# Optimization experiments

Measured on AMD Instinct MI355X. Metric: run time of the kernel, lower is better.

Reference implementation:

```python
import jax, jax.numpy as jnp
import numpy as np

L = 6  # num_objects (greedy iterations)
BIG = 1e8  # penalty for already-used template ids (matches torch code)


def setup_inputs() -> dict:
    key = jax.random.key(0)
    k1, k2, k3, k4 = jax.random.split(key, 4)
    B, T, C, H, W = 16, 144, 1, 128, 128
    x = jax.random.uniform(k1, (B, C, H, W), jnp.float32)
    templates = jax.random.uniform(k2, (B, T, C, H, W), jnp.float32)
    masks = jax.random.uniform(k3, (B, T, 1, H, W), jnp.float32)
    background = jax.random.uniform(k4, (1, C, H, W), jnp.float32)
    return {"x": x, "templates": templates, "masks": masks, "background": background}


def _greedy_select(x, templates, masks, background):
    """Greedy template selection. Faithful to DecompModel._greedy_selection
    (use_empty is falsy by default -> empty template = 5*ones, empty mask = ones).
    Key identity used for efficiency: dead-leaves composition of the l
    already-selected objects is affine in whatever lies below them:
        recons = A + Mprod * below,
    where A accumulates painted objects and Mprod = prod(1 - mask_i).
    The new candidate at step l is painted BELOW the existing selection
    (it sits at the last index, and compose_templates paints last->first),
    so below = cand*cand_mask + bg*(1-cand_mask). Identical math, no
    O(B*T*l) recomposition per step."""
    B, T = templates.shape[0], templates.shape[1]
    H, W = templates.shape[-2], templates.shape[-1]
    empty_t = 5.0 * jnp.ones((B, 1) + templates.shape[2:], templates.dtype)
    empty_m = jnp.ones((B, 1) + masks.shape[2:], masks.dtype)
    temps = jnp.concatenate([empty_t, templates], axis=1)   # (B,T+1,C,H,W)
    ms = jnp.concatenate([empty_m, masks], axis=1)           # (B,T+1,1,H,W)
    bg = jnp.broadcast_to(background, (B,) + background.shape[1:])  # (B,C,H,W)

    A0 = jnp.zeros_like(bg)                                  # painted-so-far
    M0 = jnp.ones((B, 1, H, W), bg.dtype)                    # transmission
    used0 = jnp.zeros((B, T + 1), bool)
    bidx = jnp.arange(B)

    def step(carry, _):
        A, Mprod, used = carry
        below = temps * ms + bg[:, None] * (1.0 - ms)        # (B,T+1,C,H,W)
        recons = A[:, None] + Mprod[:, None] * below         # (B,T+1,C,H,W)
        errors = jnp.mean((x[:, None] - recons) ** 2, axis=(2, 3, 4))  # (B,T+1)
        errors = jnp.where(used, BIG, errors)
        ids = jnp.argmin(errors, axis=1)                     # (B,)
        hit = (jnp.arange(T + 1)[None, :] == ids[:, None]) & (ids[:, None] != 0)
        used = used | hit                                    # empty id=0 reusable
        sel_t = temps[bidx, ids]                             # (B,C,H,W)
        sel_m = ms[bidx, ids]                                # (B,1,H,W)
        A = A + Mprod * sel_t * sel_m
        Mprod = Mprod * (1.0 - sel_m)
        return (A, Mprod, used), ids

    (_, _, _), ids = jax.lax.scan(step, (A0, M0, used0), None, length=L)
    ids = ids.T                                              # (B,L)
    objects = temps[bidx[:, None], ids]                      # (B,L,C,H,W)
    omasks = ms[bidx[:, None], ids]                          # (B,L,1,H,W)
    return objects, omasks, ids


def _compose(objects, omasks, background):
    """Dead-leaves composition, painting from last object to first
    (first selected object ends up on top), as in compose_templates."""
    B, N = objects.shape[0], objects.shape[1]
    recons = jnp.broadcast_to(background, (B,) + background.shape[1:])
    for i in range(N):  # small fixed loop over L objects
        o = objects[:, N - 1 - i]
        m = omasks[:, N - 1 - i]
        recons = o * m + recons * (1.0 - m)
    return recons


def reference(x, templates, masks, background):
    objects, omasks, ids = _greedy_select(x, templates, masks, background)
    recons = _compose(objects, omasks, background)           # (B,C,H,W)
    return recons, objects, omasks, ids
```

## Files before the change

### kernel.cpp

```cpp
#include <hip/hip_runtime.h>

#define BB 16
#define TT 144
#define TP1 145
#define HWP 16384
#define HW4 4096
#define LL 6
#define BIGE 1e30

typedef float f4 __attribute__((ext_vector_type(4)));

static const size_t OFF_A     = 0;
static const size_t OFF_M     = 1048576;
static const size_t OFF_U     = 2097152;
static const size_t OFF_V     = 3145728;
static const size_t OFF_ERR   = 4194304;
static const size_t OFF_USED  = 4227072;
static const size_t OFF_BELOW = 4259840;
static const size_t WS_FULL   = OFF_BELOW + 150994944ull;

__device__ __forceinline__ float hsum(f4 v) { return ((v.x + v.y) + v.z) + v.w; }

__device__ __forceinline__ double blk_reduce(double s) {
    for (int off = 32; off; off >>= 1) s += __shfl_down(s, off);
    __shared__ double smr[4];
    if ((threadIdx.x & 63) == 0) smr[threadIdx.x >> 6] = s;
    __syncthreads();
    return smr[0] + smr[1] + smr[2] + smr[3];
}

__global__ void k_below_err0(const f4* __restrict__ temps, const f4* __restrict__ masks,
                             const f4* __restrict__ bg, const f4* __restrict__ x,
                             f4* __restrict__ below, double* __restrict__ err,
                             int* __restrict__ used) {
    const int t = blockIdx.x, b = blockIdx.y, tid = threadIdx.x;
    const f4* xb = x + (size_t)b * HW4;
    double s = 0.0;
    if (t == 0) {
        if (tid < TP1) used[b * TP1 + tid] = 0;
        for (int j = tid; j < HW4; j += 256) {
            f4 xv = xb[j];
            s += (double)(100.f - 10.f * hsum(xv));
        }
    } else {
        const size_t row = ((size_t)(b * TT + t - 1)) * HW4;
        for (int j = tid; j < HW4; j += 256) {
            f4 tv = __builtin_nontemporal_load(&temps[row + j]);
            f4 mv = __builtin_nontemporal_load(&masks[row + j]);
            f4 bv = bg[j], xv = xb[j];
            f4 w = tv * mv + bv * (1.f - mv);
            below[row + j] = w;
            f4 g = w * (w - 2.f * xv);
            s += (double)hsum(g);
        }
    }
    double tot = blk_reduce(s);
    if (tid == 0) err[b * TP1 + t] = tot;
}

template <int MODE>
__global__ void k_err(const f4* __restrict__ below,
                      const f4* __restrict__ temps, const f4* __restrict__ masks,
                      const f4* __restrict__ bg,
                      const f4* __restrict__ u, const f4* __restrict__ v,
                      const int* __restrict__ used, double* __restrict__ err) {
    const int t = blockIdx.x, b = blockIdx.y, tid = threadIdx.x;
    if (t != 0 && used[b * TP1 + t]) {
        if (tid == 0) err[b * TP1 + t] = BIGE;
        return;
    }
    const f4* ub = u + (size_t)b * HW4;
    const f4* vb = v + (size_t)b * HW4;
    double s = 0.0;
    if (t == 0) {
        for (int j = tid; j < HW4; j += 256) {
            f4 uu = ub[j], vv = vb[j];
            float g = 25.f * hsum(vv) - 10.f * hsum(uu);
            s += (double)g;
        }
    } else if (MODE == 0) {
        const size_t row = ((size_t)(b * TT + t - 1)) * HW4;
        for (int j = tid; j < HW4; j += 256) {
            f4 w = below[row + j], uu = ub[j], vv = vb[j];
            f4 g = w * (vv * w - 2.f * uu);
            s += (double)hsum(g);
        }
    } else {
        const size_t row = ((size_t)(b * TT + t - 1)) * HW4;
        for (int j = tid; j < HW4; j += 256) {
            f4 tv = temps[row + j], mv = masks[row + j], bv = bg[j];
            f4 uu = ub[j], vv = vb[j];
            f4 w = tv * mv + bv * (1.f - mv);
            f4 g = w * (vv * w - 2.f * uu);
            s += (double)hsum(g);
        }
    }
    double tot = blk_reduce(s);
    if (tid == 0) err[b * TP1 + t] = tot;
}

template <bool FIRST, bool LAST>
__global__ void k_upd(const f4* __restrict__ temps, const f4* __restrict__ masks,
                      const f4* __restrict__ x, const f4* __restrict__ bg,
                      const double* __restrict__ err,
                      int* __restrict__ used, f4* __restrict__ A, f4* __restrict__ M,
                      f4* __restrict__ u, f4* __restrict__ v,
                      f4* __restrict__ out_obj, f4* __restrict__ out_msk,
                      f4* __restrict__ out_rec, float* __restrict__ out_ids, int l) {
    const int tid = threadIdx.x;
    const int gid = blockIdx.x * 256 + tid;
    const int b = gid >> 12;
    const int p = gid & (HW4 - 1);
    __shared__ int ssel;
    if (tid < 64) {
        double best = 1e301;
        int bi = TP1;
        for (int t = tid; t < TP1; t += 64) {
            double e = err[b * TP1 + t];
            if (e < best) { best = e; bi = t; }
        }
        for (int off = 32; off; off >>= 1) {
            double oe = __shfl_down(best, off);
            int    oi = __shfl_down(bi, off);
            if (oe < best || (oe == best && oi < bi)) { best = oe; bi = oi; }
        }
        if (tid == 0) ssel = bi;
    }
    __syncthreads();
    const int id = ssel;
    f4 st, sm;
    if (id == 0) {
        st = (f4){5.f, 5.f, 5.f, 5.f};
        sm = (f4){1.f, 1.f, 1.f, 1.f};
    } else {
        size_t base = ((size_t)(b * TT + id - 1)) * HW4 + p;
        st = temps[base];
        sm = masks[base];
    }
    f4 a, mp;
    if (FIRST) { a = (f4){0.f, 0.f, 0.f, 0.f}; mp = (f4){1.f, 1.f, 1.f, 1.f}; }
    else       { a = A[gid]; mp = M[gid]; }
    a = a + mp * st * sm;
    mp = mp * (1.f - sm);
    const size_t ob = ((size_t)(b * LL + l)) * HW4 + p;
    out_obj[ob] = st;
    out_msk[ob] = sm;
    if (LAST) {
        out_rec[gid] = a + mp * bg[p];
    } else {
        A[gid] = a; M[gid] = mp;
        f4 xv = x[gid];
        u[gid] = (xv - a) * mp;
        v[gid] = mp * mp;
    }
    if ((blockIdx.x & 15) == 0 && tid == 0) {
        if (id != 0) used[b * TP1 + id] = 1;
        out_ids[b * LL + l] = (float)id;
    }
}

__global__ void k_uv0(const f4* __restrict__ x, f4* __restrict__ u, f4* __restrict__ v,
                      int* __restrict__ used) {
    int gid = blockIdx.x * blockDim.x + threadIdx.x;
    if (gid < BB * TP1) used[gid] = 0;
    if (gid >= BB * HW4) return;
    u[gid] = x[gid];
    v[gid] = (f4){1.f, 1.f, 1.f, 1.f};
}

static inline void launch_upd(bool first, bool last,
                              const f4* temps, const f4* masks, const f4* x, const f4* bg,
                              const double* err, int* used, f4* A, f4* M,
                              f4* u, f4* v, f4* out_obj, f4* out_msk, f4* out_rec,
                              float* out_ids, int l, hipStream_t stream) {
    if (first)
        k_upd<true, false><<<256, 256, 0, stream>>>(temps, masks, x, bg, err, used, A, M, u, v, out_obj, out_msk, out_rec, out_ids, l);
    else if (last)
        k_upd<false, true><<<256, 256, 0, stream>>>(temps, masks, x, bg, err, used, A, M, u, v, out_obj, out_msk, out_rec, out_ids, l);
    else
        k_upd<false, false><<<256, 256, 0, stream>>>(temps, masks, x, bg, err, used, A, M, u, v, out_obj, out_msk, out_rec, out_ids, l);
}

extern "C" void kernel_launch(void* const* d_in, const int* in_sizes, int n_in,
                              void* d_out, int out_size, void* d_ws, size_t ws_size,
                              hipStream_t stream) {
    const f4* x     = (const f4*)d_in[0];
    const f4* temps = (const f4*)d_in[1];
    const f4* masks = (const f4*)d_in[2];
    const f4* bg    = (const f4*)d_in[3];

    float* out      = (float*)d_out;
    f4*    out_rec  = (f4*)out;
    f4*    out_obj  = (f4*)(out + 262144);
    f4*    out_msk  = (f4*)(out + 262144 + 1572864);
    float* out_ids  = out + 262144 + 2 * 1572864;

    char* ws = (char*)d_ws;
    f4*     A     = (f4*)(ws + OFF_A);
    f4*     M     = (f4*)(ws + OFF_M);
    f4*     u     = (f4*)(ws + OFF_U);
    f4*     v     = (f4*)(ws + OFF_V);
    double* err   = (double*)(ws + OFF_ERR);
    int*    used  = (int*)(ws + OFF_USED);
    f4*     below = (f4*)(ws + OFF_BELOW);

    const bool full = (ws_size >= WS_FULL);

    if (full) {
        k_below_err0<<<dim3(TP1, BB), 256, 0, stream>>>(temps, masks, bg, x, below, err, used);
        for (int l = 0; l < LL; ++l) {
            launch_upd(l == 0, l == LL - 1, temps, masks, x, bg, err, used, A, M, u, v,
                       out_obj, out_msk, out_rec, out_ids, l, stream);
            if (l < LL - 1)
                k_err<0><<<dim3(TP1, BB), 256, 0, stream>>>(
                    below, nullptr, nullptr, nullptr, u, v, used, err);
        }
    } else {
        k_uv0<<<(BB * HW4 + 255) / 256, 256, 0, stream>>>(x, u, v, used);
        for (int l = 0; l < LL; ++l) {
            k_err<1><<<dim3(TP1, BB), 256, 0, stream>>>(
                nullptr, temps, masks, bg, u, v, used, err);
            launch_upd(l == 0, l == LL - 1, temps, masks, x, bg, err, used, A, M, u, v,
                       out_obj, out_msk, out_rec, out_ids, l, stream);
        }
    }
}
```

Baseline: 258.4 us.

## Store precomputed below in fp16 and refine near-best candidates in fp32

The cached per-candidate 'below' image is now stored as half precision, which halves the traffic of the per-step error sweep. A second kernel takes the fp16 error estimates and recomputes, in fp32 from the original templates and masks, only those candidates whose estimate lies within an error-bound margin of the minimum. All other candidates get a large sentinel, so selection should match the fp32 result as long as the margin bound holds. This adds one extra launch per step and depends on the heuristic margin being wide enough to keep the true argmin.

```diff
diff --git a/kernel.cpp b/kernel.cpp
--- a/kernel.cpp
+++ b/kernel.cpp
@@ -1,25 +1,35 @@
 #include <hip/hip_runtime.h>
+#include <math.h>
 
 #define BB 16
 #define TT 144
 #define TP1 145
 #define HWP 16384
 #define HW4 4096
+#define HW8 2048
 #define LL 6
 #define BIGE 1e30
 
-typedef float f4 __attribute__((ext_vector_type(4)));
+typedef float     f4 __attribute__((ext_vector_type(4)));
+typedef float     f8 __attribute__((ext_vector_type(8)));
+typedef _Float16  h4 __attribute__((ext_vector_type(4)));
+typedef _Float16  h8 __attribute__((ext_vector_type(8)));
 
 static const size_t OFF_A     = 0;
-static const size_t OFF_M     = 1048576;
-static const size_t OFF_U     = 2097152;
-static const size_t OFF_V     = 3145728;
-static const size_t OFF_ERR   = 4194304;
-static const size_t OFF_USED  = 4227072;
-static const size_t OFF_BELOW = 4259840;
-static const size_t WS_FULL   = OFF_BELOW + 150994944ull;
+static const size_t OFF_M     = 1u << 20;
+static const size_t OFF_U     = 2u << 20;
+static const size_t OFF_V     = 3u << 20;
+static const size_t OFF_ERR32 = 4u << 20;
+static const size_t OFF_ERR16 = (4u << 20) + 32768;
+static const size_t OFF_D     = (4u << 20) + 65536;
+static const size_t OFF_USED  = (4u << 20) + 81920;
+static const size_t OFF_B16   = (4u << 20) + 98304;
+static const size_t WS_FULL   = OFF_B16 + 75497472ull;
 
 __device__ __forceinline__ float hsum(f4 v) { return ((v.x + v.y) + v.z) + v.w; }
+__device__ __forceinline__ float hsum8(f8 v) {
+    return (((v.s0 + v.s1) + (v.s2 + v.s3)) + ((v.s4 + v.s5) + (v.s6 + v.s7)));
+}
 
 __device__ __forceinline__ double blk_reduce(double s) {
     for (int off = 32; off; off >>= 1) s += __shfl_down(s, off);
@@ -29,9 +39,18 @@
     return smr[0] + smr[1] + smr[2] + smr[3];
 }
 
+__device__ __forceinline__ void blk_reduce2(double& a, double& b) {
+    for (int off = 32; off; off >>= 1) { a += __shfl_down(a, off); b += __shfl_down(b, off); }
+    __shared__ double sa[4], sb[4];
+    if ((threadIdx.x & 63) == 0) { sa[threadIdx.x >> 6] = a; sb[threadIdx.x >> 6] = b; }
+    __syncthreads();
+    a = sa[0] + sa[1] + sa[2] + sa[3];
+    b = sb[0] + sb[1] + sb[2] + sb[3];
+}
+
 __global__ void k_below_err0(const f4* __restrict__ temps, const f4* __restrict__ masks,
                              const f4* __restrict__ bg, const f4* __restrict__ x,
-                             f4* __restrict__ below, double* __restrict__ err,
+                             h4* __restrict__ below16, double* __restrict__ err32,
                              int* __restrict__ used) {
     const int t = blockIdx.x, b = blockIdx.y, tid = threadIdx.x;
     const f4* xb = x + (size_t)b * HW4;
@@ -49,41 +68,115 @@
             f4 mv = __builtin_nontemporal_load(&masks[row + j]);
             f4 bv = bg[j], xv = xb[j];
             f4 w = tv * mv + bv * (1.f - mv);
-            below[row + j] = w;
+            below16[row + j] = __builtin_convertvector(w, h4);
             f4 g = w * (w - 2.f * xv);
             s += (double)hsum(g);
         }
     }
     double tot = blk_reduce(s);
-    if (tid == 0) err[b * TP1 + t] = tot;
-}
-
-template <int MODE>
-__global__ void k_err(const f4* __restrict__ below,
-                      const f4* __restrict__ temps, const f4* __restrict__ masks,
-                      const f4* __restrict__ bg,
-                      const f4* __restrict__ u, const f4* __restrict__ v,
-                      const int* __restrict__ used, double* __restrict__ err) {
+    if (tid == 0) err32[b * TP1 + t] = tot;
+}
+
+__global__ void k_err16(const h8* __restrict__ below16,
+                        const f4* __restrict__ u4, const f4* __restrict__ v4,
+                        const int* __restrict__ used, double* __restrict__ err16,
+                        double* __restrict__ D) {
     const int t = blockIdx.x, b = blockIdx.y, tid = threadIdx.x;
     if (t != 0 && used[b * TP1 + t]) {
-        if (tid == 0) err[b * TP1 + t] = BIGE;
-        return;
-    }
-    const f4* ub = u + (size_t)b * HW4;
-    const f4* vb = v + (size_t)b * HW4;
+        if (tid == 0) err16[b * TP1 + t] = BIGE;
+        return;
+    }
+    if (t == 0) {
+        const f4* ub = u4 + (size_t)b * HW4;
+        const f4* vb = v4 + (size_t)b * HW4;
+        double s = 0.0, d = 0.0;
+        for (int j = tid; j < HW4; j += 256) {
+            f4 uu = ub[j], vv = vb[j];
+            s += (double)(25.f * hsum(vv) - 10.f * hsum(uu));
+            f4 au = {fabsf(uu.x), fabsf(uu.y), fabsf(uu.z), fabsf(uu.w)};
+            d += (double)hsum(vv + au);
+        }
+        blk_reduce2(s, d);
+        if (tid == 0) { err16[b * TP1] = s; D[b] = d; }
+        return;
+    }
+    const f8* ub = (const f8*)(u4 + (size_t)b * HW4);
+    const f8* vb = (const f8*)(v4 + (size_t)b * HW4);
+    const h8* wb = below16 + ((size_t)(b * TT + t - 1)) * HW8;
+    double s = 0.0;
+    for (int j = tid; j < HW8; j += 256) {
+        f8 w = __builtin_convertvector(wb[j], f8);
+        f8 uu = ub[j], vv = vb[j];
+        f8 g = w * (vv * w - 2.f * uu);
+        s += (double)hsum8(g);
+    }
+    double tot = blk_reduce(s);
+    if (tid == 0) err16[b * TP1 + t] = tot;
+}
+
+__global__ void k_refine(const f4* __restrict__ temps, const f4* __restrict__ masks,
+                         const f4* __restrict__ bg,
+                         const f4* __restrict__ u4, const f4* __restrict__ v4,
+                         const double* __restrict__ err16, const double* __restrict__ D,
+                         double* __restrict__ err32) {
+    const int t = blockIdx.x, b = blockIdx.y, tid = threadIdx.x;
+    double e = (tid < TP1) ? err16[b * TP1 + tid] : 1e300;
+    for (int off = 32; off; off >>= 1) {
+        double oe = __shfl_down(e, off);
+        e = (oe < e) ? oe : e;
+    }
+    __shared__ double sm[4];
+    __shared__ double smin_s;
+    if ((tid & 63) == 0) sm[tid >> 6] = e;
+    __syncthreads();
+    if (tid == 0) {
+        double m0 = (sm[0] < sm[1]) ? sm[0] : sm[1];
+        double m1 = (sm[2] < sm[3]) ? sm[2] : sm[3];
+        smin_s = (m0 < m1) ? m0 : m1;
+    }
+    __syncthreads();
+    const double smin = smin_s;
+    const double mine = err16[b * TP1 + t];
+    const double margin = 2.0 * (1.0e-3 * D[b] + 0.25);
+    if (mine > smin + margin) {
+        if (tid == 0) err32[b * TP1 + t] = BIGE;
+        return;
+    }
+    if (t == 0) {
+        if (tid == 0) err32[b * TP1 + t] = mine;
+        return;
+    }
+    const f4* ub = u4 + (size_t)b * HW4;
+    const f4* vb = v4 + (size_t)b * HW4;
+    const size_t row = ((size_t)(b * TT + t - 1)) * HW4;
+    double s = 0.0;
+    for (int j = tid; j < HW4; j += 256) {
+        f4 tv = temps[row + j], mv = masks[row + j], bv = bg[j];
+        f4 uu = ub[j], vv = vb[j];
+        f4 w = tv * mv + bv * (1.f - mv);
+        f4 g = w * (vv * w - 2.f * uu);
+        s += (double)hsum(g);
+    }
+    double tot = blk_reduce(s);
+    if (tid == 0) err32[b * TP1 + t] = tot;
+}
+
+__global__ void k_err_f32(const f4* __restrict__ temps, const f4* __restrict__ masks,
+                          const f4* __restrict__ bg,
+                          const f4* __restrict__ u4, const f4* __restrict__ v4,
+                          const int* __restrict__ used, double* __restrict__ err32) {
+    const int t = blockIdx.x, b = blockIdx.y, tid = threadIdx.x;
+    if (t != 0 && used[b * TP1 + t]) {
+        if (tid == 0) err32[b * TP1 + t] = BIGE;
+        return;
+    }
+    const f4* ub = u4 + (size_t)b * HW4;
+    const f4* vb = v4 + (size_t)b * HW4;
     double s = 0.0;
     if (t == 0) {
         for (int j = tid; j < HW4; j += 256) {
             f4 uu = ub[j], vv = vb[j];
-            float g = 25.f * hsum(vv) - 10.f * hsum(uu);
-            s += (double)g;
-        }
-    } else if (MODE == 0) {
-        const size_t row = ((size_t)(b * TT + t - 1)) * HW4;
-        for (int j = tid; j < HW4; j += 256) {
-            f4 w = below[row + j], uu = ub[j], vv = vb[j];
-            f4 g = w * (vv * w - 2.f * uu);
-            s += (double)hsum(g);
+            s += (double)(25.f * hsum(vv) - 10.f * hsum(uu));
         }
     } else {
         const size_t row = ((size_t)(b * TT + t - 1)) * HW4;
@@ -96,7 +189,7 @@
         }
     }
     double tot = blk_reduce(s);
-    if (tid == 0) err[b * TP1 + t] = tot;
+    if (tid == 0) err32[b * TP1 + t] = tot;
 }
 
 template <bool FIRST, bool LAST>
@@ -200,27 +293,29 @@
     f4*     M     = (f4*)(ws + OFF_M);
     f4*     u     = (f4*)(ws + OFF_U);
     f4*     v     = (f4*)(ws + OFF_V);
-    double* err   = (double*)(ws + OFF_ERR);
+    double* err32 = (double*)(ws + OFF_ERR32);
+    double* err16 = (double*)(ws + OFF_ERR16);
+    double* D     = (double*)(ws + OFF_D);
     int*    used  = (int*)(ws + OFF_USED);
-    f4*     below = (f4*)(ws + OFF_BELOW);
+    h4*     b16   = (h4*)(ws + OFF_B16);
 
     const bool full = (ws_size >= WS_FULL);
 
     if (full) {
-        k_below_err0<<<dim3(TP1, BB), 256, 0, stream>>>(temps, masks, bg, x, below, err, used);
+        k_below_err0<<<dim3(TP1, BB), 256, 0, stream>>>(temps, masks, bg, x, b16, err32, used);
         for (int l = 0; l < LL; ++l) {
-            launch_upd(l == 0, l == LL - 1, temps, masks, x, bg, err, used, A, M, u, v,
+            launch_upd(l == 0, l == LL - 1, temps, masks, x, bg, err32, used, A, M, u, v,
                        out_obj, out_msk, out_rec, out_ids, l, stream);
-            if (l < LL - 1)
-                k_err<0><<<dim3(TP1, BB), 256, 0, stream>>>(
-                    below, nullptr, nullptr, nullptr, u, v, used, err);
+            if (l < LL - 1) {
+                k_err16<<<dim3(TP1, BB), 256, 0, stream>>>((const h8*)b16, u, v, used, err16, D);
+                k_refine<<<dim3(TP1, BB), 256, 0, stream>>>(temps, masks, bg, u, v, err16, D, err32);
+            }
         }
     } else {
         k_uv0<<<(BB * HW4 + 255) / 256, 256, 0, stream>>>(x, u, v, used);
         for (int l = 0; l < LL; ++l) {
-            k_err<1><<<dim3(TP1, BB), 256, 0, stream>>>(
-                nullptr, temps, masks, bg, u, v, used, err);
-            launch_upd(l == 0, l == LL - 1, temps, masks, x, bg, err, used, A, M, u, v,
+            k_err_f32<<<dim3(TP1, BB), 256, 0, stream>>>(temps, masks, bg, u, v, used, err32);
+            launch_upd(l == 0, l == LL - 1, temps, masks, x, bg, err32, used, A, M, u, v,
                        out_obj, out_msk, out_rec, out_ids, l, stream);
         }
     }
```

New measurement: 313.7 us. 21.4% more time.

## Fuse argmin and state update into per-candidate error kernel with ping-pong buffers

Applied to the files above, without the earlier changes.

Merges the separate update and error kernels into a single step kernel per greedy iteration. Every block redundantly recomputes the argmin over the previous errors and rebuilds A/M/u/v on the fly instead of reading stored u/v. The used-flag array is replaced by carrying the BIG sentinel forward in the error buffers, and A/M are double-buffered. The goal is fewer launches and less u/v traffic, paid for with redundant reads of the selected template and A/M in every candidate block. It also widens loads to 8-float vectors and remaps block order into chunks.

```diff
diff --git a/kernel.cpp b/kernel.cpp
--- a/kernel.cpp
+++ b/kernel.cpp
@@ -3,23 +3,26 @@
 #define BB 16
 #define TT 144
 #define TP1 145
-#define HWP 16384
-#define HW4 4096
+#define HW8 2048
 #define LL 6
 #define BIGE 1e30
-
-typedef float f4 __attribute__((ext_vector_type(4)));
-
-static const size_t OFF_A     = 0;
-static const size_t OFF_M     = 1048576;
-static const size_t OFF_U     = 2097152;
-static const size_t OFF_V     = 3145728;
-static const size_t OFF_ERR   = 4194304;
-static const size_t OFF_USED  = 4227072;
-static const size_t OFF_BELOW = 4259840;
+#define NB_STEP (BB * TP1)
+#define CHUNK 290
+
+typedef float f8 __attribute__((ext_vector_type(8)));
+
+static const size_t OFF_A0    = 0;
+static const size_t OFF_M0    = 1u << 20;
+static const size_t OFF_A1    = 2u << 20;
+static const size_t OFF_M1    = 3u << 20;
+static const size_t OFF_ERRA  = 4u << 20;
+static const size_t OFF_ERRB  = (4u << 20) + 32768;
+static const size_t OFF_BELOW = 5u << 20;
 static const size_t WS_FULL   = OFF_BELOW + 150994944ull;
 
-__device__ __forceinline__ float hsum(f4 v) { return ((v.x + v.y) + v.z) + v.w; }
+__device__ __forceinline__ float hsum8(f8 v) {
+    return (((v.s0 + v.s1) + (v.s2 + v.s3)) + ((v.s4 + v.s5) + (v.s6 + v.s7)));
+}
 
 __device__ __forceinline__ double blk_reduce(double s) {
     for (int off = 32; off; off >>= 1) s += __shfl_down(s, off);
@@ -29,199 +32,206 @@
     return smr[0] + smr[1] + smr[2] + smr[3];
 }
 
-__global__ void k_below_err0(const f4* __restrict__ temps, const f4* __restrict__ masks,
-                             const f4* __restrict__ bg, const f4* __restrict__ x,
-                             f4* __restrict__ below, double* __restrict__ err,
-                             int* __restrict__ used) {
+__device__ __forceinline__ int blk_argmin(const double* __restrict__ err_b) {
+    const int tid = threadIdx.x;
+    double e = 1e301; int idx = TP1;
+    if (tid < TP1) { e = err_b[tid]; idx = tid; }
+    for (int off = 32; off; off >>= 1) {
+        double oe = __shfl_down(e, off);
+        int    oi = __shfl_down(idx, off);
+        if (oe < e || (oe == e && oi < idx)) { e = oe; idx = oi; }
+    }
+    __shared__ double se[4]; __shared__ int si[4]; __shared__ int ssel;
+    if ((tid & 63) == 0) { se[tid >> 6] = e; si[tid >> 6] = idx; }
+    __syncthreads();
+    if (tid == 0) {
+        double be = se[0]; int bi = si[0];
+        for (int w = 1; w < 4; ++w)
+            if (se[w] < be || (se[w] == be && si[w] < bi)) { be = se[w]; bi = si[w]; }
+        ssel = bi;
+    }
+    __syncthreads();
+    return ssel;
+}
+
+template <bool STORE>
+__global__ void k_build(const f8* __restrict__ temps, const f8* __restrict__ masks,
+                        const f8* __restrict__ bg, const f8* __restrict__ x,
+                        f8* __restrict__ below, double* __restrict__ err) {
     const int t = blockIdx.x, b = blockIdx.y, tid = threadIdx.x;
-    const f4* xb = x + (size_t)b * HW4;
+    const f8* xb = x + (size_t)b * HW8;
     double s = 0.0;
     if (t == 0) {
-        if (tid < TP1) used[b * TP1 + tid] = 0;
-        for (int j = tid; j < HW4; j += 256) {
-            f4 xv = xb[j];
-            s += (double)(100.f - 10.f * hsum(xv));
-        }
+        for (int j = tid; j < HW8; j += 256)
+            s += (double)(200.f - 10.f * hsum8(xb[j]));
     } else {
-        const size_t row = ((size_t)(b * TT + t - 1)) * HW4;
-        for (int j = tid; j < HW4; j += 256) {
-            f4 tv = __builtin_nontemporal_load(&temps[row + j]);
-            f4 mv = __builtin_nontemporal_load(&masks[row + j]);
-            f4 bv = bg[j], xv = xb[j];
-            f4 w = tv * mv + bv * (1.f - mv);
-            below[row + j] = w;
-            f4 g = w * (w - 2.f * xv);
-            s += (double)hsum(g);
+        const size_t row = ((size_t)(b * TT + t - 1)) * HW8;
+        for (int j = tid; j < HW8; j += 256) {
+            f8 tv = __builtin_nontemporal_load(&temps[row + j]);
+            f8 mv = __builtin_nontemporal_load(&masks[row + j]);
+            f8 bv = bg[j], xv = xb[j];
+            f8 w = tv * mv + bv * (1.f - mv);
+            if (STORE) below[row + j] = w;
+            s += (double)hsum8(w * (w - 2.f * xv));
         }
     }
     double tot = blk_reduce(s);
     if (tid == 0) err[b * TP1 + t] = tot;
 }
 
-template <int MODE>
-__global__ void k_err(const f4* __restrict__ below,
-                      const f4* __restrict__ temps, const f4* __restrict__ masks,
-                      const f4* __restrict__ bg,
-                      const f4* __restrict__ u, const f4* __restrict__ v,
-                      const int* __restrict__ used, double* __restrict__ err) {
-    const int t = blockIdx.x, b = blockIdx.y, tid = threadIdx.x;
-    if (t != 0 && used[b * TP1 + t]) {
-        if (tid == 0) err[b * TP1 + t] = BIGE;
+template <bool FIRST, int MODE>
+__global__ void k_step(const f8* __restrict__ temps, const f8* __restrict__ masks,
+                       const f8* __restrict__ bg, const f8* __restrict__ x,
+                       const f8* __restrict__ below,
+                       const double* __restrict__ err_old, double* __restrict__ err_new,
+                       const f8* __restrict__ Aold, const f8* __restrict__ Mold,
+                       f8* __restrict__ Anew, f8* __restrict__ Mnew,
+                       f8* __restrict__ out_obj, f8* __restrict__ out_msk,
+                       float* __restrict__ out_ids, int slot) {
+    const int lin = blockIdx.x;
+    const int wg  = (lin & 7) * CHUNK + (lin >> 3);
+    const int b   = wg / TP1;
+    const int t   = wg - b * TP1;
+    const int tid = threadIdx.x;
+
+    const int sel = blk_argmin(err_old + b * TP1);
+
+    const double my_old = err_old[b * TP1 + t];
+    const bool masked = (t != 0) && (t == sel || my_old >= 0.5 * BIGE);
+    if (masked) {
+        if (tid == 0) err_new[b * TP1 + t] = BIGE;
         return;
     }
-    const f4* ub = u + (size_t)b * HW4;
-    const f4* vb = v + (size_t)b * HW4;
+
+    const bool selzero = (sel == 0);
+    const size_t selrow = selzero ? 0 : ((size_t)(b * TT + sel - 1)) * HW8;
+    const size_t rowt   = (t > 0) ? ((size_t)(b * TT + t - 1)) * HW8 : 0;
+    const f8* xb = x + (size_t)b * HW8;
+    const f8* Ab = Aold + (size_t)b * HW8;
+    const f8* Mb = Mold + (size_t)b * HW8;
+    const size_t ob = ((size_t)(b * LL + slot)) * HW8;
+    const bool writer = (t == 0);
+
     double s = 0.0;
-    if (t == 0) {
-        for (int j = tid; j < HW4; j += 256) {
-            f4 uu = ub[j], vv = vb[j];
-            float g = 25.f * hsum(vv) - 10.f * hsum(uu);
-            s += (double)g;
+    for (int j = tid; j < HW8; j += 256) {
+        f8 st, sm;
+        if (selzero) { st = (f8)(5.f); sm = (f8)(1.f); }
+        else         { st = temps[selrow + j]; sm = masks[selrow + j]; }
+        f8 a, mp;
+        if (FIRST) { a = (f8)(0.f); mp = (f8)(1.f); }
+        else       { a = Ab[j]; mp = Mb[j]; }
+        a = a + mp * st * sm;
+        mp = mp * (1.f - sm);
+        if (writer) {
+            Anew[(size_t)b * HW8 + j] = a;
+            Mnew[(size_t)b * HW8 + j] = mp;
+            out_obj[ob + j] = st;
+            out_msk[ob + j] = sm;
         }
-    } else if (MODE == 0) {
-        const size_t row = ((size_t)(b * TT + t - 1)) * HW4;
-        for (int j = tid; j < HW4; j += 256) {
-            f4 w = below[row + j], uu = ub[j], vv = vb[j];
-            f4 g = w * (vv * w - 2.f * uu);
-            s += (double)hsum(g);
+        f8 xv = xb[j];
+        f8 u = (xv - a) * mp;
+        f8 v = mp * mp;
+        if (t == 0) {
+            s += (double)hsum8(25.f * v - 10.f * u);
+        } else {
+            f8 w;
+            if (MODE == 0) w = below[rowt + j];
+            else {
+                f8 tv = temps[rowt + j], mv = masks[rowt + j];
+                w = tv * mv + bg[j] * (1.f - mv);
+            }
+            s += (double)hsum8(w * (v * w - 2.f * u));
         }
-    } else {
-        const size_t row = ((size_t)(b * TT + t - 1)) * HW4;
-        for (int j = tid; j < HW4; j += 256) {
-            f4 tv = temps[row + j], mv = masks[row + j], bv = bg[j];
-            f4 uu = ub[j], vv = vb[j];
-            f4 w = tv * mv + bv * (1.f - mv);
-            f4 g = w * (vv * w - 2.f * uu);
-            s += (double)hsum(g);
-        }
     }
     double tot = blk_reduce(s);
-    if (tid == 0) err[b * TP1 + t] = tot;
-}
-
-template <bool FIRST, bool LAST>
-__global__ void k_upd(const f4* __restrict__ temps, const f4* __restrict__ masks,
-                      const f4* __restrict__ x, const f4* __restrict__ bg,
-                      const double* __restrict__ err,
-                      int* __restrict__ used, f4* __restrict__ A, f4* __restrict__ M,
-                      f4* __restrict__ u, f4* __restrict__ v,
-                      f4* __restrict__ out_obj, f4* __restrict__ out_msk,
-                      f4* __restrict__ out_rec, float* __restrict__ out_ids, int l) {
+    if (tid == 0) {
+        err_new[b * TP1 + t] = tot;
+        if (writer) out_ids[b * LL + slot] = (float)sel;
+    }
+}
+
+__global__ void k_final(const f8* __restrict__ temps, const f8* __restrict__ masks,
+                        const f8* __restrict__ bg,
+                        const double* __restrict__ err_old,
+                        const f8* __restrict__ Aold, const f8* __restrict__ Mold,
+                        f8* __restrict__ out_rec, f8* __restrict__ out_obj,
+                        f8* __restrict__ out_msk, float* __restrict__ out_ids) {
     const int tid = threadIdx.x;
     const int gid = blockIdx.x * 256 + tid;
-    const int b = gid >> 12;
-    const int p = gid & (HW4 - 1);
-    __shared__ int ssel;
-    if (tid < 64) {
-        double best = 1e301;
-        int bi = TP1;
-        for (int t = tid; t < TP1; t += 64) {
-            double e = err[b * TP1 + t];
-            if (e < best) { best = e; bi = t; }
-        }
-        for (int off = 32; off; off >>= 1) {
-            double oe = __shfl_down(best, off);
-            int    oi = __shfl_down(bi, off);
-            if (oe < best || (oe == best && oi < bi)) { best = oe; bi = oi; }
-        }
-        if (tid == 0) ssel = bi;
-    }
-    __syncthreads();
-    const int id = ssel;
-    f4 st, sm;
-    if (id == 0) {
-        st = (f4){5.f, 5.f, 5.f, 5.f};
-        sm = (f4){1.f, 1.f, 1.f, 1.f};
-    } else {
-        size_t base = ((size_t)(b * TT + id - 1)) * HW4 + p;
-        st = temps[base];
-        sm = masks[base];
-    }
-    f4 a, mp;
-    if (FIRST) { a = (f4){0.f, 0.f, 0.f, 0.f}; mp = (f4){1.f, 1.f, 1.f, 1.f}; }
-    else       { a = A[gid]; mp = M[gid]; }
+    const int b = gid >> 11;
+    const int j = gid & (HW8 - 1);
+
+    const int sel = blk_argmin(err_old + b * TP1);
+
+    f8 st, sm;
+    if (sel == 0) { st = (f8)(5.f); sm = (f8)(1.f); }
+    else {
+        size_t base = ((size_t)(b * TT + sel - 1)) * HW8 + j;
+        st = temps[base]; sm = masks[base];
+    }
+    f8 a = Aold[(size_t)b * HW8 + j], mp = Mold[(size_t)b * HW8 + j];
     a = a + mp * st * sm;
     mp = mp * (1.f - sm);
-    const size_t ob = ((size_t)(b * LL + l)) * HW4 + p;
+    const size_t ob = ((size_t)(b * LL + (LL - 1))) * HW8 + j;
     out_obj[ob] = st;
     out_msk[ob] = sm;
-    if (LAST) {
-        out_rec[gid] = a + mp * bg[p];
-    } else {
-        A[gid] = a; M[gid] = mp;
-        f4 xv = x[gid];
-        u[gid] = (xv - a) * mp;
-        v[gid] = mp * mp;
-    }
-    if ((blockIdx.x & 15) == 0 && tid == 0) {
-        if (id != 0) used[b * TP1 + id] = 1;
-        out_ids[b * LL + l] = (float)id;
-    }
-}
-
-__global__ void k_uv0(const f4* __restrict__ x, f4* __restrict__ u, f4* __restrict__ v,
-                      int* __restrict__ used) {
-    int gid = blockIdx.x * blockDim.x + threadIdx.x;
-    if (gid < BB * TP1) used[gid] = 0;
-    if (gid >= BB * HW4) return;
-    u[gid] = x[gid];
-    v[gid] = (f4){1.f, 1.f, 1.f, 1.f};
-}
-
-static inline void launch_upd(bool first, bool last,
-                              const f4* temps, const f4* masks, const f4* x, const f4* bg,
-                              const double* err, int* used, f4* A, f4* M,
-                              f4* u, f4* v, f4* out_obj, f4* out_msk, f4* out_rec,
-                              float* out_ids, int l, hipStream_t stream) {
-    if (first)
-        k_upd<true, false><<<256, 256, 0, stream>>>(temps, masks, x, bg, err, used, A, M, u, v, out_obj, out_msk, out_rec, out_ids, l);
-    else if (last)
-        k_upd<false, true><<<256, 256, 0, stream>>>(temps, masks, x, bg, err, used, A, M, u, v, out_obj, out_msk, out_rec, out_ids, l);
-    else
-        k_upd<false, false><<<256, 256, 0, stream>>>(temps, masks, x, bg, err, used, A, M, u, v, out_obj, out_msk, out_rec, out_ids, l);
+    out_rec[(size_t)b * HW8 + j] = a + mp * bg[j];
+    if (tid == 0 && (blockIdx.x & 7) == 0)
+        out_ids[b * LL + (LL - 1)] = (float)sel;
 }
 
 extern "C" void kernel_launch(void* const* d_in, const int* in_sizes, int n_in,
                               void* d_out, int out_size, void* d_ws, size_t ws_size,
                               hipStream_t stream) {
-    const f4* x     = (const f4*)d_in[0];
-    const f4* temps = (const f4*)d_in[1];
-    const f4* masks = (const f4*)d_in[2];
-    const f4* bg    = (const f4*)d_in[3];
+    const f8* x     = (const f8*)d_in[0];
+    const f8* temps = (const f8*)d_in[1];
+    const f8* masks = (const f8*)d_in[2];
+    const f8* bg    = (const f8*)d_in[3];
 
     float* out      = (float*)d_out;
-    f4*    out_rec  = (f4*)out;
-    f4*    out_obj  = (f4*)(out + 262144);
-    f4*    out_msk  = (f4*)(out + 262144 + 1572864);
+    f8*    out_rec  = (f8*)out;
+    f8*    out_obj  = (f8*)(out + 262144);
+    f8*    out_msk  = (f8*)(out + 262144 + 1572864);
     float* out_ids  = out + 262144 + 2 * 1572864;
 
     char* ws = (char*)d_ws;
-    f4*     A     = (f4*)(ws + OFF_A);
-    f4*     M     = (f4*)(ws + OFF_M);
-    f4*     u     = (f4*)(ws + OFF_U);
-    f4*     v     = (f4*)(ws + OFF_V);
-    double* err   = (double*)(ws + OFF_ERR);
-    int*    used  = (int*)(ws + OFF_USED);
-    f4*     below = (f4*)(ws + OFF_BELOW);
+    f8*     A0    = (f8*)(ws + OFF_A0);
+    f8*     M0    = (f8*)(ws + OFF_M0);
+    f8*     A1    = (f8*)(ws + OFF_A1);
+    f8*     M1    = (f8*)(ws + OFF_M1);
+    double* errA  = (double*)(ws + OFF_ERRA);
+    double* errB  = (double*)(ws + OFF_ERRB);
+    f8*     below = (f8*)(ws + OFF_BELOW);
 
     const bool full = (ws_size >= WS_FULL);
 
     if (full) {
-        k_below_err0<<<dim3(TP1, BB), 256, 0, stream>>>(temps, masks, bg, x, below, err, used);
-        for (int l = 0; l < LL; ++l) {
-            launch_upd(l == 0, l == LL - 1, temps, masks, x, bg, err, used, A, M, u, v,
-                       out_obj, out_msk, out_rec, out_ids, l, stream);
-            if (l < LL - 1)
-                k_err<0><<<dim3(TP1, BB), 256, 0, stream>>>(
-                    below, nullptr, nullptr, nullptr, u, v, used, err);
-        }
+        k_build<true><<<dim3(TP1, BB), 256, 0, stream>>>(temps, masks, bg, x, below, errA);
+        k_step<true, 0><<<NB_STEP, 256, 0, stream>>>(temps, masks, bg, x, below,
+            errA, errB, nullptr, nullptr, A0, M0, out_obj, out_msk, out_ids, 0);
+        k_step<false, 0><<<NB_STEP, 256, 0, stream>>>(temps, masks, bg, x, below,
+            errB, errA, A0, M0, A1, M1, out_obj, out_msk, out_ids, 1);
+        k_step<false, 0><<<NB_STEP, 256, 0, stream>>>(temps, masks, bg, x, below,
+            errA, errB, A1, M1, A0, M0, out_obj, out_msk, out_ids, 2);
+        k_step<false, 0><<<NB_STEP, 256, 0, stream>>>(temps, masks, bg, x, below,
+            errB, errA, A0, M0, A1, M1, out_obj, out_msk, out_ids, 3);
+        k_step<false, 0><<<NB_STEP, 256, 0, stream>>>(temps, masks, bg, x, below,
+            errA, errB, A1, M1, A0, M0, out_obj, out_msk, out_ids, 4);
+        k_final<<<128, 256, 0, stream>>>(temps, masks, bg, errB, A0, M0,
+            out_rec, out_obj, out_msk, out_ids);
     } else {
-        k_uv0<<<(BB * HW4 + 255) / 256, 256, 0, stream>>>(x, u, v, used);
-        for (int l = 0; l < LL; ++l) {
-            k_err<1><<<dim3(TP1, BB), 256, 0, stream>>>(
-                nullptr, temps, masks, bg, u, v, used, err);
-            launch_upd(l == 0, l == LL - 1, temps, masks, x, bg, err, used, A, M, u, v,
-                       out_obj, out_msk, out_rec, out_ids, l, stream);
-        }
-    }
-}
+        k_build<false><<<dim3(TP1, BB), 256, 0, stream>>>(temps, masks, bg, x, nullptr, errA);
+        k_step<true, 1><<<NB_STEP, 256, 0, stream>>>(temps, masks, bg, x, nullptr,
+            errA, errB, nullptr, nullptr, A0, M0, out_obj, out_msk, out_ids, 0);
+        k_step<false, 1><<<NB_STEP, 256, 0, stream>>>(temps, masks, bg, x, nullptr,
+            errB, errA, A0, M0, A1, M1, out_obj, out_msk, out_ids, 1);
+        k_step<false, 1><<<NB_STEP, 256, 0, stream>>>(temps, masks, bg, x, nullptr,
+            errA, errB, A1, M1, A0, M0, out_obj, out_msk, out_ids, 2);
+        k_step<false, 1><<<NB_STEP, 256, 0, stream>>>(temps, masks, bg, x, nullptr,
+            errB, errA, A0, M0, A1, M1, out_obj, out_msk, out_ids, 3);
+        k_step<false, 1><<<NB_STEP, 256, 0, stream>>>(temps, masks, bg, x, nullptr,
+            errA, errB, A1, M1, A0, M0, out_obj, out_msk, out_ids, 4);
+        k_final<<<128, 256, 0, stream>>>(temps, masks, bg, errB, A0, M0,
+            out_rec, out_obj, out_msk, out_ids);
+    }
+}
```

Measured after the change: 319.9 us. +23.8%, slower.
